# Performance work log

Hardware: AMD Instinct MI355X
Metric: run time of the kernel (lower is better)

Reference implementation:

```python
import jax, jax.numpy as jnp
import numpy as np

N = 50000
E = 1600000
D = 128
NUM_CLASSES = 10
SLOPE = 0.01  # torch leaky_relu default


def leaky_relu(x):
    return jnp.where(x >= 0, x, SLOPE * x)


def gcn_conv(x, src, dst, norm_out, norm_in, W, b):
    # DGL GraphConv, norm='both': D_out^{-1/2} A^T D_in^{-1/2} applied as
    # scale-src -> scatter-sum to dst -> scale-dst, then linear + bias.
    h = x * norm_out[:, None]                        # [N, D]
    agg = jax.ops.segment_sum(h[src], dst, num_segments=N)  # [N, D]
    agg = agg * norm_in[:, None]
    return agg @ W + b


def setup_inputs() -> dict:
    key = jax.random.key(0)
    ks = jax.random.split(key, 12)
    def w(k, shape, fan_in):
        return jax.random.normal(k, shape, dtype=jnp.float32) / np.sqrt(fan_in)
    return {
        "x": jax.random.normal(ks[0], (N, D), dtype=jnp.float32),
        "src": jax.random.randint(ks[1], (E,), 0, N),
        "dst": jax.random.randint(ks[2], (E,), 0, N),
        "W1": w(ks[3], (D, D), D),
        "b1": jnp.zeros((D,), jnp.float32),
        "W2": w(ks[4], (D, D), D),
        "b2": jnp.zeros((D,), jnp.float32),
        "agg_w": w(ks[5], (D, 1), D),
        "agg_b": jnp.zeros((1,), jnp.float32),
        "d1_w": w(ks[6], (N, 100), N),
        "d1_b": jnp.zeros((100,), jnp.float32),
        "d2_w": w(ks[7], (100, 20), 100),
        "d2_b": jnp.zeros((20,), jnp.float32),
        "d3_w": w(ks[8], (20, NUM_CLASSES), 20),
        "d3_b": jnp.zeros((NUM_CLASSES,), jnp.float32),
    }


def reference(x, src, dst, W1, b1, W2, b2, agg_w, agg_b,
              d1_w, d1_b, d2_w, d2_b, d3_w, d3_b):
    ones = jnp.ones((E,), jnp.float32)
    out_deg = jax.ops.segment_sum(ones, src, num_segments=N)
    in_deg = jax.ops.segment_sum(ones, dst, num_segments=N)
    # DGL clamps degrees to min 1 (allow_zero_in_degree path)
    norm_out = jnp.power(jnp.clip(out_deg, 1.0), -0.5)
    norm_in = jnp.power(jnp.clip(in_deg, 1.0), -0.5)

    h = gcn_conv(x, src, dst, norm_out, norm_in, W1, b1)
    h = leaky_relu(h)
    h = gcn_conv(h, src, dst, norm_out, norm_in, W2, b2)
    h = h @ agg_w + agg_b            # [N, 1]
    # dropout omitted (eval mode / identity)
    h = h.reshape(-1, N)             # [1, N]
    h = h @ d1_w + d1_b              # [1, 100]
    h = leaky_relu(h @ d2_w + d2_b)  # [1, 20]
    h = h @ d3_w + d3_b              # [1, num_classes]
    return h.reshape(1, -1)
```

## Files before the change

kernel.cpp:

```cpp
#include <hip/hip_runtime.h>
#include <hip/hip_bf16.h>

#define SLOPE 0.01f
#define D 128
#define CAP 64
#define NB 1024
#define KE 7
#define SBUF (KE * 256)
#define NRMAX 64
#define HBK 256
#define HBINSB 50176
#define HWB (HBINSB / 4)
#define ZB 512
#define ZIT 10

__device__ __forceinline__ float us2f(unsigned int u) {
    union { unsigned int i; float f; } c; c.i = u << 16; return c.f;
}
__device__ __forceinline__ unsigned int f2us(float f) {
    union { float f; unsigned int i; } c; c.f = f;
    return (c.i + 0x7fffu + ((c.i >> 16) & 1u)) >> 16;
}

__global__ void __launch_bounds__(256) k_hista(const int* __restrict__ src,
                                               unsigned int* __restrict__ hist,
                                               int E, int N, int npass) {
    __shared__ unsigned int lh[HWB];
    int b = blockIdx.x;
    int chunk = (E + gridDim.x - 1) / gridDim.x;
    int e0 = b * chunk, e1 = min(E, e0 + chunk);
    int base = 0;
    for (int p = 0; p < npass; p++, base += HBINSB) {
        for (int i = threadIdx.x; i < HWB; i += 256) lh[i] = 0;
        __syncthreads();
        for (int e = e0 + threadIdx.x; e < e1; e += 256) {
            unsigned int r = (unsigned int)(src[e] - base);
            if (r < HBINSB) atomicAdd(&lh[r >> 2], 1u << ((r & 3u) << 3));
        }
        __syncthreads();
        unsigned int* outp = hist + ((size_t)b * npass + p) * HWB;
        for (int i = threadIdx.x; i < HWB; i += 256) outp[i] = lh[i];
        __syncthreads();
    }
}

__global__ void k_norm(const unsigned int* __restrict__ hist,
                       float* __restrict__ norm_out, int N, int npass) {
    int i = blockIdx.x * blockDim.x + threadIdx.x;
    if (i >= N) return;
    int p = i / HBINSB;
    int ib = i - p * HBINSB;
    int w = ib >> 2, sh = (ib & 3) << 3;
    unsigned int dsum = 0;
    for (int b = 0; b < HBK; b++)
        dsum += (hist[((size_t)b * npass + p) * HWB + w] >> sh) & 0xffu;
    norm_out[i] = rsqrtf(fmaxf((float)dsum, 1.0f));
}

__global__ void __launch_bounds__(256) k_histc(const int* __restrict__ dst,
                                               unsigned int* __restrict__ histg,
                                               int E, int NR) {
    __shared__ int lb[NRMAX];
    int b = blockIdx.x;
    if (threadIdx.x < NRMAX) lb[threadIdx.x] = 0;
    __syncthreads();
    int ch = (E + NB - 1) / NB;
    int e0 = b * ch, e1 = min(E, e0 + ch);
    for (int e = e0 + threadIdx.x; e < e1; e += 256) atomicAdd(&lb[dst[e] >> 10], 1);
    __syncthreads();
    unsigned int* row = histg + (size_t)b * NRMAX;
    if (threadIdx.x < NRMAX) row[threadIdx.x] = (unsigned int)lb[threadIdx.x];
}

__global__ void __launch_bounds__(NB) k_scanA(const unsigned int* __restrict__ histg,
                                              unsigned int* __restrict__ boffT,
                                              unsigned int* __restrict__ tot, int NR) {
    __shared__ int wsum[NB / 64];
    int p = blockIdx.x, tid = threadIdx.x, lane = tid & 63, w = tid >> 6;
    int val = (int)histg[(size_t)tid * NRMAX + p];
    int sc = val;
    for (int off = 1; off < 64; off <<= 1) { int t = __shfl_up(sc, off, 64); if (lane >= off) sc += t; }
    if (lane == 63) wsum[w] = sc;
    __syncthreads();
    if (w == 0 && lane < NB / 64) {
        int v4 = wsum[lane];
        for (int off = 1; off < NB / 64; off <<= 1) { int t = __shfl_up(v4, off, 64); if (lane >= off) v4 += t; }
        wsum[lane] = v4;
    }
    __syncthreads();
    int excl = ((w == 0) ? 0 : wsum[w - 1]) + sc - val;
    boffT[(size_t)p * NB + tid] = (unsigned int)excl;
    if (tid == NB - 1) tot[p] = (unsigned int)(excl + val);
}

__global__ void __launch_bounds__(1024) k_misc(const unsigned int* __restrict__ tot,
                                               int* __restrict__ rbase, int NR,
                                               const float* __restrict__ W2, const float* __restrict__ b2,
                                               const float* __restrict__ agg_w, const float* __restrict__ agg_b,
                                               float* __restrict__ v, float* __restrict__ c) {
    __shared__ int wsum[16];
    __shared__ float aw[D];
    __shared__ float red[D];
    int tid = threadIdx.x;
    if (blockIdx.x == 0) {
        int lane = tid & 63, w = tid >> 6;
        int val = (tid < NR) ? (int)tot[tid] : 0;
        int sc = val;
        for (int off = 1; off < 64; off <<= 1) { int t = __shfl_up(sc, off, 64); if (lane >= off) sc += t; }
        if (lane == 63) wsum[w] = sc;
        __syncthreads();
        if (w == 0 && lane < 16) {
            int v16 = wsum[lane];
            for (int off = 1; off < 16; off <<= 1) { int t = __shfl_up(v16, off, 64); if (lane >= off) v16 += t; }
            wsum[lane] = v16;
        }
        __syncthreads();
        int excl = ((w == 0) ? 0 : wsum[w - 1]) + sc - val;
        if (tid <= NR) rbase[tid] = excl;
    } else {
        if (tid >= 128) return;
        aw[tid] = agg_w[tid];
        __syncthreads();
        float acc = 0.f;
        for (int j = 0; j < D; j++) acc += W2[tid * D + j] * aw[j];
        v[tid] = acc;
        red[tid] = b2[tid] * aw[tid];
        __syncthreads();
        for (int off = 64; off > 0; off >>= 1) {
            if (tid < off) red[tid] += red[tid + off];
            __syncthreads();
        }
        if (tid == 0) c[0] = red[0] + agg_b[0];
    }
}

__global__ void __launch_bounds__(256) k_psort(const int* __restrict__ src, const int* __restrict__ dst,
                                               const int* __restrict__ rbase,
                                               const unsigned int* __restrict__ boffT,
                                               unsigned int* __restrict__ parted, int E, int NR) {
    __shared__ int lhist[NRMAX];
    __shared__ int lstart[NRMAX];
    __shared__ unsigned int sbuf[SBUF];
    int b = blockIdx.x, tid = threadIdx.x;
    if (tid < NRMAX) lhist[tid] = 0;
    __syncthreads();
    int ch = (E + NB - 1) / NB;
    int e0 = b * ch, e1 = min(E, e0 + ch);

    unsigned int rec[KE];
#pragma unroll
    for (int k = 0; k < KE; k++) {
        int e = e0 + k * 256 + tid;
        rec[k] = 0xffffffffu;
        if (e < e1) {
            int d = dst[e], s = src[e];
            rec[k] = (unsigned int)s | ((unsigned int)(d & 1023) << 16) | ((unsigned int)(d >> 10) << 26);
            atomicAdd(&lhist[d >> 10], 1);
        }
    }
    __syncthreads();

    if (tid < 64) {
        int val = lhist[tid];
        int sc = val;
        for (int off = 1; off < 64; off <<= 1) { int t = __shfl_up(sc, off, 64); if (tid >= off) sc += t; }
        int ex = sc - val;
        lhist[tid] = ex;
        lstart[tid] = (tid < NR) ? (rbase[tid] + (int)boffT[(size_t)tid * NB + b] - ex) : 0;
    }
    __syncthreads();

#pragma unroll
    for (int k = 0; k < KE; k++) {
        if (rec[k] != 0xffffffffu) {
            int p = rec[k] >> 26;
            int pos = atomicAdd(&lhist[p], 1);
            sbuf[pos] = rec[k];
        }
    }
    __syncthreads();

    int totl = e1 - e0;
    for (int j = tid; j < totl; j += 256) {
        unsigned int r = sbuf[j];
        parted[lstart[r >> 26] + j] = r & 0x03ffffffu;
    }
}

__global__ void __launch_bounds__(256) k_bfill(
    const int* __restrict__ rbase, const unsigned int* __restrict__ parted,
    unsigned short* __restrict__ bucket, int* __restrict__ cnt_in,
    float* __restrict__ norm_in, int N) {
    __shared__ int lcnt[64];
    __shared__ unsigned short blds[64 * CAP];
    int p = blockIdx.x, tid = threadIdx.x;
    int r = p >> 4, pr = p & 15;
    if (tid < 64) lcnt[tid] = 0;
    unsigned int sent2 = (unsigned int)N | ((unsigned int)N << 16);
    for (int i = tid; i < 64 * CAP / 2; i += 256) ((unsigned int*)blds)[i] = sent2;
    __syncthreads();
    int e0 = rbase[r], e1 = rbase[r + 1];
    for (int i = e0 + tid; i < e1; i += 256) {
        unsigned int rec = parted[i];
        int nl = (rec >> 16) & 1023;
        if ((nl >> 6) == pr) {
            int dl = nl & 63;
            int pos = atomicAdd(&lcnt[dl], 1);
            if (pos < CAP) blds[dl * CAP + pos] = (unsigned short)(rec & 0xffffu);
        }
    }
    __syncthreads();
    int nmax = min(64, N - (p << 6));
    unsigned int* bg = (unsigned int*)(bucket + ((long)p << 6) * CAP);
    const unsigned int* bl = (const unsigned int*)blds;
    for (int i = tid; i < nmax * (CAP / 2); i += 256) bg[i] = bl[i];
    if (tid < nmax) {
        cnt_in[(p << 6) + tid] = lcnt[tid];
        norm_in[(p << 6) + tid] = rsqrtf(fmaxf((float)lcnt[tid], 1.0f));
    }
}

__global__ void k_prep(const float2* __restrict__ x2, const float* __restrict__ norm_out,
                       unsigned int* __restrict__ xb, int N) {
    int g = blockIdx.x * blockDim.x + threadIdx.x;
    int node = g >> 6;
    if (node > N) return;
    int u = g & 63;
    int pass = u >> 4, fu = u & 15;
    unsigned int outv = 0u;
    if (node < N) {
        float no = norm_out[node];
        float2 p = x2[g];
        outv = f2us(p.x * no) | (f2us(p.y * no) << 16);
    }
    xb[((size_t)pass * (N + 1) + node) * 16 + fu] = outv;
}

__global__ void __launch_bounds__(256) k_gather1(
    const int* __restrict__ cnt_in, const unsigned short* __restrict__ bucket,
    const unsigned int* __restrict__ xb, unsigned int* __restrict__ agg, int N) {
    int b = blockIdx.x;
    int xcd = b & 7;
    int pass = xcd >> 1;
    int idx = ((b >> 3) << 1) + (xcd & 1);
    int tid = threadIdx.x;
    int node = idx * 4 + (tid >> 6);
    if (node >= N) return;
    int lane = tid & 63;
    int slot = lane >> 4;
    int fu = lane & 15;
    int deg = min(__builtin_nontemporal_load(cnt_in + node), CAP);
    int myedge = (int)__builtin_nontemporal_load(bucket + (long)node * CAP + lane);
    const unsigned int* xq = xb + (size_t)pass * (N + 1) * 16 + fu;
    float ax = 0.f, ay = 0.f;
    {
        unsigned int pv[8];
#pragma unroll
        for (int i = 0; i < 8; i++) {
            int s = __shfl(myedge, i * 4 + slot, 64);
            pv[i] = xq[(size_t)s << 4];
        }
#pragma unroll
        for (int i = 0; i < 8; i++) {
            ax += us2f(pv[i] & 0xffffu);
            ay += us2f(pv[i] >> 16);
        }
    }
    if (deg > 32) {
        unsigned int pv[8];
#pragma unroll
        for (int i = 0; i < 8; i++) {
            int s = __shfl(myedge, 32 + i * 4 + slot, 64);
            pv[i] = xq[(size_t)s << 4];
        }
#pragma unroll
        for (int i = 0; i < 8; i++) {
            ax += us2f(pv[i] & 0xffffu);
            ay += us2f(pv[i] >> 16);
        }
    }
    ax += __shfl_xor(ax, 16, 64); ay += __shfl_xor(ay, 16, 64);
    ax += __shfl_xor(ax, 32, 64); ay += __shfl_xor(ay, 32, 64);
    if (slot == 0)
        __builtin_nontemporal_store(f2us(ax) | (f2us(ay) << 16),
                                    agg + (long)node * 64 + (pass << 4) + fu);
}

__global__ void __launch_bounds__(256) k_lin1q(
    const unsigned int* __restrict__ agg, const float* __restrict__ W1,
    const float* __restrict__ b1, const float* __restrict__ v,
    const float* __restrict__ norm_out, const float* __restrict__ norm_in,
    float* __restrict__ q, int N) {
    __shared__ __align__(16) unsigned int at[64 * 64];
    int tid = threadIdx.x;
    int cg = tid & 31;
    int rg = tid >> 5;
    int r0 = blockIdx.x * 64;

    {
        const uint4* ag4 = (const uint4*)agg;
        uint4* at4 = (uint4*)at;
        uint4 z4; z4.x = z4.y = z4.z = z4.w = 0u;
#pragma unroll
        for (int it = 0; it < 4; it++) {
            int idx = tid + it * 256;
            int r = idx >> 4;
            at4[idx] = (r0 + r < N) ? ag4[(long)(r0 + r) * 16 + (idx & 15)] : z4;
        }
    }
    __syncthreads();

    float4 acc[8];
#pragma unroll
    for (int i = 0; i < 8; i++) acc[i].x = acc[i].y = acc[i].z = acc[i].w = 0.f;

    const float4* W4 = (const float4*)W1;
    const uint4* a4 = ((const uint4*)at) + rg * 8 * 16;
    for (int kq = 0; kq < 16; kq++) {
        float4 w0 = W4[(kq * 8 + 0) * 32 + cg];
        float4 w1 = W4[(kq * 8 + 1) * 32 + cg];
        float4 w2 = W4[(kq * 8 + 2) * 32 + cg];
        float4 w3 = W4[(kq * 8 + 3) * 32 + cg];
        float4 w4 = W4[(kq * 8 + 4) * 32 + cg];
        float4 w5 = W4[(kq * 8 + 5) * 32 + cg];
        float4 w6 = W4[(kq * 8 + 6) * 32 + cg];
        float4 w7 = W4[(kq * 8 + 7) * 32 + cg];
#pragma unroll
        for (int i = 0; i < 8; i++) {
            uint4 a = a4[i * 16 + kq];
            float f0 = us2f(a.x & 0xffffu), f1 = us2f(a.x >> 16);
            float f2 = us2f(a.y & 0xffffu), f3 = us2f(a.y >> 16);
            float f4 = us2f(a.z & 0xffffu), f5 = us2f(a.z >> 16);
            float f6 = us2f(a.w & 0xffffu), f7 = us2f(a.w >> 16);
            acc[i].x += f0*w0.x + f1*w1.x + f2*w2.x + f3*w3.x + f4*w4.x + f5*w5.x + f6*w6.x + f7*w7.x;
            acc[i].y += f0*w0.y + f1*w1.y + f2*w2.y + f3*w3.y + f4*w4.y + f5*w5.y + f6*w6.y + f7*w7.y;
            acc[i].z += f0*w0.z + f1*w1.z + f2*w2.z + f3*w3.z + f4*w4.z + f5*w5.z + f6*w6.z + f7*w7.z;
            acc[i].w += f0*w0.w + f1*w1.w + f2*w2.w + f3*w3.w + f4*w4.w + f5*w5.w + f6*w6.w + f7*w7.w;
        }
    }

    float4 bv = ((const float4*)b1)[cg];
    float4 vv = ((const float4*)v)[cg];
#pragma unroll
    for (int i = 0; i < 8; i++) {
        int row = r0 + rg * 8 + i;
        bool valid = row < N;
        float ni = valid ? norm_in[row] : 0.f;
        float hx = ni * acc[i].x + bv.x; hx = hx >= 0.f ? hx : SLOPE * hx;
        float hy = ni * acc[i].y + bv.y; hy = hy >= 0.f ? hy : SLOPE * hy;
        float hz = ni * acc[i].z + bv.z; hz = hz >= 0.f ? hz : SLOPE * hz;
        float hw = ni * acc[i].w + bv.w; hw = hw >= 0.f ? hw : SLOPE * hw;
        float p = hx * vv.x + hy * vv.y + hz * vv.z + hw * vv.w;
        p += __shfl_down(p, 16, 32);
        p += __shfl_down(p, 8, 32);
        p += __shfl_down(p, 4, 32);
        p += __shfl_down(p, 2, 32);
        p += __shfl_down(p, 1, 32);
        if ((tid & 31) == 0 && valid)
            q[row] = norm_out[row] * p;
    }
}

__global__ void __launch_bounds__(256) k_gather2(
    const int* __restrict__ cnt_in, const unsigned short* __restrict__ bucket,
    const float* __restrict__ q, const float* __restrict__ norm_in,
    const float* __restrict__ c, float* __restrict__ s, int N) {
    int tid = threadIdx.x;
    int node = blockIdx.x * 8 + (tid >> 5);
    int lane = tid & 31;
    if (node >= N) return;
    int deg = min(cnt_in[node], CAP);
    float t = 0.f;
    for (int j = lane; j < deg; j += 32) t += q[(int)bucket[(long)node * CAP + j]];
    t += __shfl_down(t, 16, 32);
    t += __shfl_down(t, 8, 32);
    t += __shfl_down(t, 4, 32);
    t += __shfl_down(t, 2, 32);
    t += __shfl_down(t, 1, 32);
    if (lane == 0) s[node] = norm_in[node] * t + c[0];
}

__global__ void __launch_bounds__(256) k_z1(const float* __restrict__ s,
                                            const float* __restrict__ d1w,
                                            float* __restrict__ zpart, int N) {
    __shared__ float ls[ZIT * 10];
    __shared__ float4 part[256];
    int tid = threadIdx.x;
    int qd = tid % 25;
    int rl = tid / 25;
    int rows_per = (N + gridDim.x - 1) / gridDim.x;
    int r0 = blockIdx.x * rows_per;
    int r1 = min(N, r0 + rows_per);
    if (tid < ZIT * 10) ls[tid] = (r0 + tid < r1) ? s[r0 + tid] : 0.f;
    __syncthreads();
    const float4* w4 = (const float4*)d1w;
    float4 acc; acc.x = acc.y = acc.z = acc.w = 0.f;
    if (tid < 250) {
#pragma unroll
        for (int it = 0; it < ZIT; it++) {
            int ro = rl + it * 10;
            float sv = ls[ro];
            int rr = min(r0 + ro, N - 1);
            float4 w = w4[(long)rr * 25 + qd];
            acc.x += sv * w.x; acc.y += sv * w.y; acc.z += sv * w.z; acc.w += sv * w.w;
        }
    }
    part[tid] = acc;
    __syncthreads();
    if (tid < 25) {
        float4 t = part[tid];
#pragma unroll
        for (int g = 1; g < 10; g++) {
            float4 p = part[tid + 25 * g];
            t.x += p.x; t.y += p.y; t.z += p.z; t.w += p.w;
        }
        ((float4*)zpart)[blockIdx.x * 25 + tid] = t;
    }
}

__global__ void __launch_bounds__(1024) k_tail(const float* __restrict__ zpart,
                                               const float* __restrict__ d1b,
                                               const float* __restrict__ d2w, const float* __restrict__ d2b,
                                               const float* __restrict__ d3w, const float* __restrict__ d3b,
                                               float* __restrict__ out) {
    __shared__ float z1c[100];
    __shared__ float z2c[20];
    int tid = threadIdx.x;
    if (tid < 100) z1c[tid] = 0.f;
    __syncthreads();
    if (tid < 1000) {
        int col = tid % 100;
        int bg = tid / 100;
        float acc = 0.f;
        for (int b = bg; b < ZB; b += 10) acc += zpart[(size_t)b * 100 + col];
        atomicAdd(&z1c[col], acc);
    }
    __syncthreads();
    if (tid < 100) z1c[tid] += d1b[tid];
    __syncthreads();
    if (tid < 20) {
        float acc = d2b[tid];
        for (int k = 0; k < 100; k++) acc += z1c[k] * d2w[k * 20 + tid];
        z2c[tid] = acc >= 0.f ? acc : SLOPE * acc;
    }
    __syncthreads();
    if (tid < 10) {
        float acc = d3b[tid];
        for (int j = 0; j < 20; j++) acc += z2c[j] * d3w[j * 10 + tid];
        out[tid] = acc;
    }
}

extern "C" void kernel_launch(void* const* d_in, const int* in_sizes, int n_in,
                              void* d_out, int out_size, void* d_ws, size_t ws_size,
                              hipStream_t stream) {
    const int N = in_sizes[0] / D;
    const int E = in_sizes[1];
    const int NP = (N + 63) >> 6;
    const int NR = (N + 1023) >> 10;
    const int npass = (N + HBINSB - 1) / HBINSB;

    const float* x     = (const float*)d_in[0];
    const int* src     = (const int*)d_in[1];
    const int* dst     = (const int*)d_in[2];
    const float* W1    = (const float*)d_in[3];
    const float* b1    = (const float*)d_in[4];
    const float* W2    = (const float*)d_in[5];
    const float* b2    = (const float*)d_in[6];
    const float* agg_w = (const float*)d_in[7];
    const float* agg_b = (const float*)d_in[8];
    const float* d1w   = (const float*)d_in[9];
    const float* d1b   = (const float*)d_in[10];
    const float* d2w   = (const float*)d_in[11];
    const float* d2b   = (const float*)d_in[12];
    const float* d3w   = (const float*)d_in[13];
    const float* d3b   = (const float*)d_in[14];
    float* out = (float*)d_out;

    unsigned int* xb  = (unsigned int*)d_ws;
    unsigned int* histg  = xb;
    unsigned int* boffT  = histg + (size_t)NB * NRMAX;
    unsigned int* tot    = boffT + (size_t)NRMAX * NB;
    unsigned int* histA  = tot + 128;
    unsigned int* agg = xb + (size_t)(N + 1) * 64;
    unsigned int* parted = agg;
    float* norm_out   = (float*)(agg + (size_t)N * 64);
    float* norm_in    = norm_out + N;
    float* q          = norm_in + N;
    float* s          = q + N;
    float* v          = s + N;
    float* c          = v + 128;
    int* rbase        = (int*)(c + 4);
    int* cnt_in       = rbase + NRMAX + 16;
    unsigned short* bucket = (unsigned short*)(cnt_in + N);
    float* zpart      = (float*)(bucket + (size_t)N * CAP);

    k_hista<<<HBK, 256, 0, stream>>>(src, histA, E, N, npass);
    k_histc<<<NB, 256, 0, stream>>>(dst, histg, E, NR);
    k_scanA<<<NR, NB, 0, stream>>>(histg, boffT, tot, NR);
    k_misc<<<2, 1024, 0, stream>>>(tot, rbase, NR, W2, b2, agg_w, agg_b, v, c);
    k_norm<<<(N + 255) / 256, 256, 0, stream>>>(histA, norm_out, N, npass);
    k_psort<<<NB, 256, 0, stream>>>(src, dst, rbase, boffT, parted, E, NR);
    k_bfill<<<NP, 256, 0, stream>>>(rbase, parted, bucket, cnt_in, norm_in, N);
    k_prep<<<((N + 1) * 64 + 255) / 256, 256, 0, stream>>>((const float2*)x, norm_out, xb, N);

    {
        const int G = (N + 3) / 4;
        const int G2 = (G + 1) / 2;
        k_gather1<<<8 * G2, 256, 0, stream>>>(cnt_in, bucket, xb, agg, N);
    }
    k_lin1q<<<(N + 63) / 64, 256, 0, stream>>>(agg, W1, b1, v, norm_out, norm_in, q, N);
    k_gather2<<<(N + 7) / 8, 256, 0, stream>>>(cnt_in, bucket, q, norm_in, c, s, N);
    k_z1<<<ZB, 256, 0, stream>>>(s, d1w, zpart, N);
    k_tail<<<1, 1024, 0, stream>>>(zpart, d1b, d2w, d2b, d3w, d3b, out);
}
```

Before: 372.9 us.

## Use finer 256-node dst partitions and two-pass 8-byte gather

Changes the dst partitioning from 1024-node ranges to 256-node ranges, so each bucket-fill block scans a quarter as many partitioned edges. The 64-entry scans in psort are replaced by a two-level 256-entry scan. Separately, the first gather now splits the 128 features into two halves instead of four and loads 8 bytes per lane, which halves the number of gather passes over the edge lists. The cost is larger per-pass feature slices per node and bigger histogram and offset tables.

```diff
diff --git a/kernel.cpp b/kernel.cpp
--- a/kernel.cpp
+++ b/kernel.cpp
@@ -7,7 +7,7 @@
 #define NB 1024
 #define KE 7
 #define SBUF (KE * 256)
-#define NRMAX 64
+#define NRMAX 256
 #define HBK 256
 #define HBINSB 50176
 #define HWB (HBINSB / 4)
@@ -62,14 +62,14 @@
                                                int E, int NR) {
     __shared__ int lb[NRMAX];
     int b = blockIdx.x;
-    if (threadIdx.x < NRMAX) lb[threadIdx.x] = 0;
+    lb[threadIdx.x] = 0;
     __syncthreads();
     int ch = (E + NB - 1) / NB;
     int e0 = b * ch, e1 = min(E, e0 + ch);
-    for (int e = e0 + threadIdx.x; e < e1; e += 256) atomicAdd(&lb[dst[e] >> 10], 1);
+    for (int e = e0 + threadIdx.x; e < e1; e += 256) atomicAdd(&lb[dst[e] >> 8], 1);
     __syncthreads();
     unsigned int* row = histg + (size_t)b * NRMAX;
-    if (threadIdx.x < NRMAX) row[threadIdx.x] = (unsigned int)lb[threadIdx.x];
+    row[threadIdx.x] = (unsigned int)lb[threadIdx.x];
 }
 
 __global__ void __launch_bounds__(NB) k_scanA(const unsigned int* __restrict__ histg,
@@ -141,8 +141,9 @@
     __shared__ int lhist[NRMAX];
     __shared__ int lstart[NRMAX];
     __shared__ unsigned int sbuf[SBUF];
-    int b = blockIdx.x, tid = threadIdx.x;
-    if (tid < NRMAX) lhist[tid] = 0;
+    __shared__ int wsum[4];
+    int b = blockIdx.x, tid = threadIdx.x, lane = tid & 63, w = tid >> 6;
+    lhist[tid] = 0;
     __syncthreads();
     int ch = (E + NB - 1) / NB;
     int e0 = b * ch, e1 = min(E, e0 + ch);
@@ -154,26 +155,33 @@
         rec[k] = 0xffffffffu;
         if (e < e1) {
             int d = dst[e], s = src[e];
-            rec[k] = (unsigned int)s | ((unsigned int)(d & 1023) << 16) | ((unsigned int)(d >> 10) << 26);
-            atomicAdd(&lhist[d >> 10], 1);
-        }
-    }
-    __syncthreads();
-
-    if (tid < 64) {
-        int val = lhist[tid];
-        int sc = val;
-        for (int off = 1; off < 64; off <<= 1) { int t = __shfl_up(sc, off, 64); if (tid >= off) sc += t; }
-        int ex = sc - val;
-        lhist[tid] = ex;
-        lstart[tid] = (tid < NR) ? (rbase[tid] + (int)boffT[(size_t)tid * NB + b] - ex) : 0;
-    }
+            rec[k] = (unsigned int)s | ((unsigned int)(d & 255) << 16) | ((unsigned int)(d >> 8) << 24);
+            atomicAdd(&lhist[d >> 8], 1);
+        }
+    }
+    __syncthreads();
+
+    int val = lhist[tid];
+    int sc = val;
+    for (int off = 1; off < 64; off <<= 1) { int t = __shfl_up(sc, off, 64); if (lane >= off) sc += t; }
+    if (lane == 63) wsum[w] = sc;
+    __syncthreads();
+    if (w == 0 && lane < 4) {
+        int vv = wsum[lane];
+        for (int off = 1; off < 4; off <<= 1) { int t = __shfl_up(vv, off, 64); if (lane >= off) vv += t; }
+        wsum[lane] = vv;
+    }
+    __syncthreads();
+    int excl = ((w == 0) ? 0 : wsum[w - 1]) + sc - val;
+    int gb = (tid < NR) ? (rbase[tid] + (int)boffT[(size_t)tid * NB + b] - excl) : 0;
+    lhist[tid] = excl;
+    lstart[tid] = gb;
     __syncthreads();
 
 #pragma unroll
     for (int k = 0; k < KE; k++) {
         if (rec[k] != 0xffffffffu) {
-            int p = rec[k] >> 26;
+            int p = rec[k] >> 24;
             int pos = atomicAdd(&lhist[p], 1);
             sbuf[pos] = rec[k];
         }
@@ -183,7 +191,7 @@
     int totl = e1 - e0;
     for (int j = tid; j < totl; j += 256) {
         unsigned int r = sbuf[j];
-        parted[lstart[r >> 26] + j] = r & 0x03ffffffu;
+        parted[lstart[r >> 24] + j] = r & 0x00ffffffu;
     }
 }
 
@@ -194,7 +202,7 @@
     __shared__ int lcnt[64];
     __shared__ unsigned short blds[64 * CAP];
     int p = blockIdx.x, tid = threadIdx.x;
-    int r = p >> 4, pr = p & 15;
+    int r = p >> 2, pr = p & 3;
     if (tid < 64) lcnt[tid] = 0;
     unsigned int sent2 = (unsigned int)N | ((unsigned int)N << 16);
     for (int i = tid; i < 64 * CAP / 2; i += 256) ((unsigned int*)blds)[i] = sent2;
@@ -202,7 +210,7 @@
     int e0 = rbase[r], e1 = rbase[r + 1];
     for (int i = e0 + tid; i < e1; i += 256) {
         unsigned int rec = parted[i];
-        int nl = (rec >> 16) & 1023;
+        int nl = (rec >> 16) & 255;
         if ((nl >> 6) == pr) {
             int dl = nl & 63;
             int pos = atomicAdd(&lcnt[dl], 1);
@@ -226,14 +234,14 @@
     int node = g >> 6;
     if (node > N) return;
     int u = g & 63;
-    int pass = u >> 4, fu = u & 15;
+    int pass = u >> 5, fu2 = u & 31;
     unsigned int outv = 0u;
     if (node < N) {
         float no = norm_out[node];
         float2 p = x2[g];
         outv = f2us(p.x * no) | (f2us(p.y * no) << 16);
     }
-    xb[((size_t)pass * (N + 1) + node) * 16 + fu] = outv;
+    xb[((size_t)pass * (N + 1) + node) * 32 + fu2] = outv;
 }
 
 __global__ void __launch_bounds__(256) k_gather1(
@@ -241,49 +249,53 @@
     const unsigned int* __restrict__ xb, unsigned int* __restrict__ agg, int N) {
     int b = blockIdx.x;
     int xcd = b & 7;
-    int pass = xcd >> 1;
-    int idx = ((b >> 3) << 1) + (xcd & 1);
+    int pass = xcd >> 2;
+    int idx = ((b >> 3) << 2) + (xcd & 3);
     int tid = threadIdx.x;
     int node = idx * 4 + (tid >> 6);
     if (node >= N) return;
     int lane = tid & 63;
     int slot = lane >> 4;
-    int fu = lane & 15;
+    int fq = lane & 15;
     int deg = min(__builtin_nontemporal_load(cnt_in + node), CAP);
     int myedge = (int)__builtin_nontemporal_load(bucket + (long)node * CAP + lane);
-    const unsigned int* xq = xb + (size_t)pass * (N + 1) * 16 + fu;
-    float ax = 0.f, ay = 0.f;
+    const uint2* xq = (const uint2*)(xb + (size_t)pass * (N + 1) * 32) + fq;
+    float ax0 = 0.f, ay0 = 0.f, ax1 = 0.f, ay1 = 0.f;
     {
-        unsigned int pv[8];
+        uint2 pv[8];
 #pragma unroll
         for (int i = 0; i < 8; i++) {
             int s = __shfl(myedge, i * 4 + slot, 64);
-            pv[i] = xq[(size_t)s << 4];
+            pv[i] = xq[(size_t)s * 16];
         }
 #pragma unroll
         for (int i = 0; i < 8; i++) {
-            ax += us2f(pv[i] & 0xffffu);
-            ay += us2f(pv[i] >> 16);
+            ax0 += us2f(pv[i].x & 0xffffu); ay0 += us2f(pv[i].x >> 16);
+            ax1 += us2f(pv[i].y & 0xffffu); ay1 += us2f(pv[i].y >> 16);
         }
     }
     if (deg > 32) {
-        unsigned int pv[8];
+        uint2 pv[8];
 #pragma unroll
         for (int i = 0; i < 8; i++) {
             int s = __shfl(myedge, 32 + i * 4 + slot, 64);
-            pv[i] = xq[(size_t)s << 4];
+            pv[i] = xq[(size_t)s * 16];
         }
 #pragma unroll
         for (int i = 0; i < 8; i++) {
-            ax += us2f(pv[i] & 0xffffu);
-            ay += us2f(pv[i] >> 16);
-        }
-    }
-    ax += __shfl_xor(ax, 16, 64); ay += __shfl_xor(ay, 16, 64);
-    ax += __shfl_xor(ax, 32, 64); ay += __shfl_xor(ay, 32, 64);
-    if (slot == 0)
-        __builtin_nontemporal_store(f2us(ax) | (f2us(ay) << 16),
-                                    agg + (long)node * 64 + (pass << 4) + fu);
+            ax0 += us2f(pv[i].x & 0xffffu); ay0 += us2f(pv[i].x >> 16);
+            ax1 += us2f(pv[i].y & 0xffffu); ay1 += us2f(pv[i].y >> 16);
+        }
+    }
+    ax0 += __shfl_xor(ax0, 16, 64); ay0 += __shfl_xor(ay0, 16, 64);
+    ax1 += __shfl_xor(ax1, 16, 64); ay1 += __shfl_xor(ay1, 16, 64);
+    ax0 += __shfl_xor(ax0, 32, 64); ay0 += __shfl_xor(ay0, 32, 64);
+    ax1 += __shfl_xor(ax1, 32, 64); ay1 += __shfl_xor(ay1, 32, 64);
+    if (slot == 0) {
+        unsigned int* op = agg + (long)node * 64 + pass * 32 + fq * 2;
+        __builtin_nontemporal_store(f2us(ax0) | (f2us(ay0) << 16), op);
+        __builtin_nontemporal_store(f2us(ax1) | (f2us(ay1) << 16), op + 1);
+    }
 }
 
 __global__ void __launch_bounds__(256) k_lin1q(
@@ -457,7 +469,7 @@
     const int N = in_sizes[0] / D;
     const int E = in_sizes[1];
     const int NP = (N + 63) >> 6;
-    const int NR = (N + 1023) >> 10;
+    const int NR = (N + 255) >> 8;
     const int npass = (N + HBINSB - 1) / HBINSB;
 
     const float* x     = (const float*)d_in[0];
@@ -481,7 +493,7 @@
     unsigned int* histg  = xb;
     unsigned int* boffT  = histg + (size_t)NB * NRMAX;
     unsigned int* tot    = boffT + (size_t)NRMAX * NB;
-    unsigned int* histA  = tot + 128;
+    unsigned int* histA  = tot + 256;
     unsigned int* agg = xb + (size_t)(N + 1) * 64;
     unsigned int* parted = agg;
     float* norm_out   = (float*)(agg + (size_t)N * 64);
@@ -506,8 +518,8 @@
 
     {
         const int G = (N + 3) / 4;
-        const int G2 = (G + 1) / 2;
-        k_gather1<<<8 * G2, 256, 0, stream>>>(cnt_in, bucket, xb, agg, N);
+        const int G4 = (G + 3) / 4;
+        k_gather1<<<8 * G4, 256, 0, stream>>>(cnt_in, bucket, xb, agg, N);
     }
     k_lin1q<<<(N + 63) / 64, 256, 0, stream>>>(agg, W1, b1, v, norm_out, norm_in, q, N);
     k_gather2<<<(N + 7) / 8, 256, 0, stream>>>(cnt_in, bucket, q, norm_in, c, s, N);
```

New measurement: 312.1 us. 16.3% less time.
